# Kernel optimization log

Hardware: AMD Instinct MI355X
Metric: run time of the kernel (lower is better)

The kernel has to match this reference:

```python
import jax, jax.numpy as jnp
import numpy as np

N_MICS = 8
REF_MIC = 0
DIAG_LOAD = 1e-5
PI_ITERS = 30  # power-iteration steps for principal eigenvector of Phi_nn^-1 Phi_ss


def setup_inputs() -> dict:
    key = jax.random.key(0)
    k1, k2, k3, k4 = jax.random.split(key, 4)
    B, M, F, T = 8, N_MICS, 257, 2000
    return {
        "spec_re": jax.random.normal(k1, (B, M, F, T), dtype=jnp.float32),
        "spec_im": jax.random.normal(k2, (B, M, F, T), dtype=jnp.float32),
        "speech_mask": jax.random.uniform(k3, (B, F, T), dtype=jnp.float32),
        "noise_mask": jax.random.uniform(k4, (B, F, T), dtype=jnp.float32),
    }


def _mvdr(spec_re, spec_im, speech_mask, noise_mask):
    # (B, M, F, T) complex STFT -> (B, F, M, T) for per-(batch, freq) processing
    Y = (spec_re + 1j * spec_im).astype(jnp.complex64)
    Y = jnp.transpose(Y, (0, 2, 1, 3))  # (B, F, M, T)
    M = Y.shape[2]

    def masked_cov(mask):  # mask: (B, F, T) real
        msum = mask.sum(-1) + 1e-8                       # (B, F)
        Yw = Y * mask[:, :, None, :]                      # (B, F, M, T)
        Phi = jnp.einsum('bfmt,bfnt->bfmn', Yw, Y.conj())  # (B, F, M, M)
        return Phi / msum[..., None, None]

    Phi_ss = masked_cov(speech_mask)
    eye = jnp.eye(M, dtype=jnp.complex64)
    Phi_nn = masked_cov(noise_mask) + DIAG_LOAD * eye

    Phi_nn_inv = jnp.linalg.inv(Phi_nn)                   # batched (B, F, M, M)
    G = jnp.einsum('bfmn,bfnk->bfmk', Phi_nn_inv, Phi_ss)

    # Principal eigenvector of G via power iteration (G has real, nonnegative
    # eigenvalues since it is similar to a Hermitian-PSD generalized pencil),
    # matching torch.linalg.eig + argmax(eigenvalues.real) up to scale.
    v = jnp.ones(G.shape[:-1], dtype=jnp.complex64)       # (B, F, M)
    for _ in range(PI_ITERS):
        v = jnp.einsum('bfmn,bfn->bfm', G, v)
        v = v / (jnp.linalg.norm(v, axis=-1, keepdims=True) + 1e-12)

    # Relative transfer function normalized to reference mic (removes scale)
    rtf = v / (v[..., REF_MIC:REF_MIC + 1] + 1e-8)        # (B, F, M)

    d = jnp.einsum('bfmn,bfn->bfm', Phi_nn_inv, rtf)      # Phi_nn^-1 rtf
    denom = jnp.einsum('bfm,bfm->bf', rtf.conj(), d).real + 1e-8
    w = d / denom[..., None]                              # (B, F, M) MVDR weights

    enhanced = jnp.einsum('bfm,bfmt->bft', w.conj(), Y)   # (B, F, T) complex
    return enhanced


def reference(spec_re, spec_im, speech_mask, noise_mask):
    return _mvdr(spec_re, spec_im, speech_mask, noise_mask)
```

## Files before the change

kernel.cpp:

```cpp
#include <hip/hip_runtime.h>

#define B_DIM 8
#define M_MICS 8
#define F_DIM 257
#define T_DIM 2000
#define NPROB (B_DIM * F_DIM)

__device__ float g_w[NPROB * 16];


#define PAIR_ACC(mq, nq, k)                                             \
    {                                                                   \
        const float pr = yr[mq][u] * yr[nq][u] + yi[mq][u] * yi[nq][u]; \
        const float pi = yi[mq][u] * yr[nq][u] - yr[mq][u] * yi[nq][u]; \
        acc[(k) + 0] += msv[u] * pr;                                    \
        acc[(k) + 1] += msv[u] * pi;                                    \
        acc[(k) + 2] += mnv[u] * pr;                                    \
        acc[(k) + 3] += mnv[u] * pi;                                    \
    }

__launch_bounds__(256, 2)
__global__ void cov_solve_kernel(const float* __restrict__ sre, const float* __restrict__ sim,
                                 const float* __restrict__ smask, const float* __restrict__ nmask)
{
    const int f = blockIdx.x, b = blockIdx.y, tid = threadIdx.x;
    const int h = tid >> 6, l = tid & 63;

    __shared__ float sG[4][34];

    const size_t mrow = (size_t)F_DIM * T_DIM;
    const size_t base_bf = ((size_t)(b * M_MICS) * F_DIM + f) * T_DIM;
    const size_t mbase   = ((size_t)b * F_DIM + f) * T_DIM;

    float acc[34];
#pragma unroll
    for (int i = 0; i < 34; ++i) acc[i] = 0.f;

#pragma unroll 1
    for (int it = 0; it < 16; ++it) {
        const int t0 = 2 * l + 128 * it;
        if (t0 < T_DIM) {
            float yr[8][2], yi[8][2];
#pragma unroll
            for (int m = 0; m < 8; ++m) {
                const float2 vr = *reinterpret_cast<const float2*>(sre + base_bf + (size_t)m * mrow + t0);
                const float2 vi = *reinterpret_cast<const float2*>(sim + base_bf + (size_t)m * mrow + t0);
                yr[m][0] = vr.x; yr[m][1] = vr.y;
                yi[m][0] = vi.x; yi[m][1] = vi.y;
            }
            const float2 ms2 = *reinterpret_cast<const float2*>(smask + mbase + t0);
            const float2 mn2 = *reinterpret_cast<const float2*>(nmask + mbase + t0);
            const float msv[2] = { ms2.x, ms2.y };
            const float mnv[2] = { mn2.x, mn2.y };

            if (h == 0) {
#pragma unroll
                for (int u = 0; u < 2; ++u) {
                    acc[0] += msv[u];
                    acc[1] += mnv[u];
#pragma unroll
                    for (int m = 0; m < 8; ++m) {
                        const float pd = yr[m][u] * yr[m][u] + yi[m][u] * yi[m][u];
                        acc[2 + m]  += msv[u] * pd;
                        acc[10 + m] += mnv[u] * pd;
                    }
                    PAIR_ACC(0, 1, 18) PAIR_ACC(0, 2, 22) PAIR_ACC(0, 3, 26) PAIR_ACC(0, 4, 30)
                }
            } else if (h == 1) {
#pragma unroll
                for (int u = 0; u < 2; ++u) {
                    PAIR_ACC(0, 5, 0)  PAIR_ACC(0, 6, 4)  PAIR_ACC(0, 7, 8)  PAIR_ACC(1, 2, 12)
                    PAIR_ACC(1, 3, 16) PAIR_ACC(1, 4, 20) PAIR_ACC(1, 5, 24) PAIR_ACC(1, 6, 28)
                }
            } else if (h == 2) {
#pragma unroll
                for (int u = 0; u < 2; ++u) {
                    PAIR_ACC(1, 7, 0)  PAIR_ACC(2, 3, 4)  PAIR_ACC(2, 4, 8)  PAIR_ACC(2, 5, 12)
                    PAIR_ACC(2, 6, 16) PAIR_ACC(2, 7, 20) PAIR_ACC(3, 4, 24) PAIR_ACC(3, 5, 28)
                }
            } else {
#pragma unroll
                for (int u = 0; u < 2; ++u) {
                    PAIR_ACC(3, 6, 0)  PAIR_ACC(3, 7, 4)  PAIR_ACC(4, 5, 8)  PAIR_ACC(4, 6, 12)
                    PAIR_ACC(4, 7, 16) PAIR_ACC(5, 6, 20) PAIR_ACC(5, 7, 24) PAIR_ACC(6, 7, 28)
                }
            }
        }
    }

#pragma unroll
    for (int i = 0; i < 34; ++i) {
        acc[i] += __shfl_xor(acc[i], 1, 64);
        acc[i] += __shfl_xor(acc[i], 2, 64);
        acc[i] += __shfl_xor(acc[i], 4, 64);
        acc[i] += __shfl_xor(acc[i], 8, 64);
        acc[i] += __shfl_xor(acc[i], 16, 64);
        acc[i] += __shfl_xor(acc[i], 32, 64);
    }
    if (l == 0) {
#pragma unroll
        for (int i = 0; i < 34; ++i) sG[h][i] = acc[i];
    }
    __syncthreads();

    if (tid < 64) {
        const int r = tid >> 3, cc = tid & 7;
        const float Ssum = sG[0][0] + 1e-8f;
        const float Nsum = sG[0][1] + 1e-8f;

        float ssr, ssi, ar, ai;
        if (r == cc) {
            ssr = sG[0][2 + r] / Ssum;  ssi = 0.f;
            ar  = sG[0][10 + r] / Nsum + 1e-5f;  ai = 0.f;
        } else {
            const int mm  = (r < cc) ? r : cc;
            const int nn2 = (r < cc) ? cc : r;
            const int q = mm * 8 - mm * (mm + 1) / 2 + nn2 - mm - 1;
            const int g = (q < 4) ? 0 : (1 + ((q - 4) >> 3));
            const int basei = (q < 4) ? (18 + 4 * q) : (4 * ((q - 4) & 7));
            const float sgn = (r < cc) ? 1.f : -1.f;
            ssr = sG[g][basei] / Ssum;
            ssi = sgn * sG[g][basei + 1] / Ssum;
            ar  = sG[g][basei + 2] / Nsum;
            ai  = sgn * sG[g][basei + 3] / Nsum;
        }

        float br = (r == cc) ? 1.f : 0.f, bi = 0.f;
        for (int k = 0; k < 8; ++k) {
            const float pr = __shfl(ar, k * 9, 64);
            const float pi = __shfl(ai, k * 9, 64);
            const float den = pr * pr + pi * pi;
            const float qr = pr / den, qi = -pi / den;
            const bool isk = (r == k);
            const float ar2 = ar * qr - ai * qi;
            const float ai2 = ar * qi + ai * qr;
            const float br2 = br * qr - bi * qi;
            const float bi2 = br * qi + bi * qr;
            ar = isk ? ar2 : ar; ai = isk ? ai2 : ai;
            br = isk ? br2 : br; bi = isk ? bi2 : bi;
            const float rar = __shfl(ar, k * 8 + cc, 64);
            const float rai = __shfl(ai, k * 8 + cc, 64);
            const float rbr = __shfl(br, k * 8 + cc, 64);
            const float rbi = __shfl(bi, k * 8 + cc, 64);
            const float fr = __shfl(ar, r * 8 + k, 64);
            const float fi = __shfl(ai, r * 8 + k, 64);
            const float uar = ar - (fr * rar - fi * rai);
            const float uai = ai - (fr * rai + fi * rar);
            const float ubr = br - (fr * rbr - fi * rbi);
            const float ubi = bi - (fr * rbi + fi * rbr);
            ar = isk ? ar : uar; ai = isk ? ai : uai;
            br = isk ? br : ubr; bi = isk ? bi : ubi;
        }

        float gr = 0.f, gi = 0.f;
        for (int k = 0; k < 8; ++k) {
            const float ir = __shfl(br, r * 8 + k, 64);
            const float ii = __shfl(bi, r * 8 + k, 64);
            const float skr = __shfl(ssr, k * 8 + cc, 64);
            const float ski = __shfl(ssi, k * 8 + cc, 64);
            gr += ir * skr - ii * ski;
            gi += ir * ski + ii * skr;
        }

        float vr = 1.f, vi = 0.f;
        for (int itp = 0; itp < 30; ++itp) {
            float wr2 = gr * vr - gi * vi;
            float wi2 = gr * vi + gi * vr;
            wr2 += __shfl_xor(wr2, 1, 64); wi2 += __shfl_xor(wi2, 1, 64);
            wr2 += __shfl_xor(wr2, 2, 64); wi2 += __shfl_xor(wi2, 2, 64);
            wr2 += __shfl_xor(wr2, 4, 64); wi2 += __shfl_xor(wi2, 4, 64);
            float nrm = wr2 * wr2 + wi2 * wi2;
            nrm += __shfl_xor(nrm, 8, 64);
            nrm += __shfl_xor(nrm, 16, 64);
            nrm += __shfl_xor(nrm, 32, 64);
            const float inv = 1.f / (sqrtf(nrm) + 1e-12f);
            wr2 *= inv; wi2 *= inv;
            vr = __shfl(wr2, cc * 9, 64);
            vi = __shfl(wi2, cc * 9, 64);
        }

        const float v0r = __shfl(vr, 0, 64) + 1e-8f;
        const float v0i = __shfl(vi, 0, 64);
        const float dd = v0r * v0r + v0i * v0i;
        const float rtr = (vr * v0r + vi * v0i) / dd;
        const float rti = (vi * v0r - vr * v0i) / dd;

        float dr = br * rtr - bi * rti;
        float di = br * rti + bi * rtr;
        dr += __shfl_xor(dr, 1, 64); di += __shfl_xor(di, 1, 64);
        dr += __shfl_xor(dr, 2, 64); di += __shfl_xor(di, 2, 64);
        dr += __shfl_xor(dr, 4, 64); di += __shfl_xor(di, 4, 64);

        float qden = (r == cc) ? (rtr * dr + rti * di) : 0.f;
        qden += __shfl_xor(qden, 1, 64); qden += __shfl_xor(qden, 2, 64);
        qden += __shfl_xor(qden, 4, 64); qden += __shfl_xor(qden, 8, 64);
        qden += __shfl_xor(qden, 16, 64); qden += __shfl_xor(qden, 32, 64);
        qden += 1e-8f;

        if (cc == 0) {
            const int p = b * F_DIM + f;
            g_w[p * 16 + r]     = dr / qden;
            g_w[p * 16 + 8 + r] = di / qden;
        }
    }
}

__launch_bounds__(256, 8)
__global__ void apply_kernel(const float* __restrict__ sre, const float* __restrict__ sim,
                             float* __restrict__ out, int out_mode)
{
    const int f = blockIdx.x, b = blockIdx.y, z = blockIdx.z;
    const int tid = threadIdx.x;
    __shared__ float sW[16];
    const int p = b * F_DIM + f;
    if (tid < 16) sW[tid] = g_w[p * 16 + tid];
    __syncthreads();

    const int t0 = z * 512 + 2 * tid;
    if (t0 >= T_DIM) return;

    const size_t mrow = (size_t)F_DIM * T_DIM;
    const size_t base_bf = ((size_t)(b * M_MICS) * F_DIM + f) * T_DIM;
    const size_t mbase   = ((size_t)b * F_DIM + f) * T_DIM;

    float er0 = 0.f, ei0 = 0.f, er1 = 0.f, ei1 = 0.f;
#pragma unroll
    for (int m = 0; m < 8; ++m) {
        const float2 vr2 = *reinterpret_cast<const float2*>(sre + base_bf + (size_t)m * mrow + t0);
        const float2 vi2 = *reinterpret_cast<const float2*>(sim + base_bf + (size_t)m * mrow + t0);
        const float wr = sW[m], wi = sW[8 + m];
        er0 += wr * vr2.x + wi * vi2.x;
        ei0 += wr * vi2.x - wi * vr2.x;
        er1 += wr * vr2.y + wi * vi2.y;
        ei1 += wr * vi2.y - wi * vr2.y;
    }
    if (out_mode == 2) {
        *reinterpret_cast<float4*>(out + 2 * (mbase + t0)) = make_float4(er0, ei0, er1, ei1);
    } else {
        *reinterpret_cast<float2*>(out + mbase + t0) = make_float2(er0, er1);
    }
}

extern "C" void kernel_launch(void* const* d_in, const int* in_sizes, int n_in,
                              void* d_out, int out_size, void* d_ws, size_t ws_size,
                              hipStream_t stream)
{
    const float* sre   = (const float*)d_in[0];
    const float* sim   = (const float*)d_in[1];
    const float* smask = (const float*)d_in[2];
    const float* nmask = (const float*)d_in[3];
    float* out = (float*)d_out;

    const int mode = (out_size >= 2 * B_DIM * F_DIM * T_DIM) ? 2 : 1;

    cov_solve_kernel<<<dim3(F_DIM, B_DIM), 256, 0, stream>>>(sre, sim, smask, nmask);
    apply_kernel<<<dim3(F_DIM, B_DIM, 4), 256, 0, stream>>>(sre, sim, out, mode);
}
```

Measured before the change: 161.1 us.

## Split covariance pair accumulation across eight waves with per-wave mic subsets

The covariance kernel now runs 512 threads (8 waves) instead of 256. Wave 0 handles the mask sums and diagonal terms, and the 28 off-diagonal mic pairs are spread four per wave over the other seven waves. Those seven waves load only the mic rows they need, using float4 loads over 4 time samples. This halves accumulator registers per thread (34 to 18) and is meant to raise occupancy and memory parallelism. The cost is redundant global (likely L2-cached) reloads of mic rows across waves, plus an imbalanced wave 0 that still loops over all 8 mics with float2 loads.

Measured after the change: 174.3 us. +8.2%, slower.

```diff
diff --git a/kernel.cpp b/kernel.cpp
--- a/kernel.cpp
+++ b/kernel.cpp
@@ -9,51 +9,79 @@
 __device__ float g_w[NPROB * 16];
 
 
-#define PAIR_ACC(mq, nq, k)                                             \
+#define PAIR_ACC(a, bb, k)                                              \
     {                                                                   \
-        const float pr = yr[mq][u] * yr[nq][u] + yi[mq][u] * yi[nq][u]; \
-        const float pi = yi[mq][u] * yr[nq][u] - yr[mq][u] * yi[nq][u]; \
+        const float pr = yr[a][u] * yr[bb][u] + yi[a][u] * yi[bb][u];   \
+        const float pi = yi[a][u] * yr[bb][u] - yr[a][u] * yi[bb][u];   \
         acc[(k) + 0] += msv[u] * pr;                                    \
         acc[(k) + 1] += msv[u] * pi;                                    \
         acc[(k) + 2] += mnv[u] * pr;                                    \
         acc[(k) + 3] += mnv[u] * pi;                                    \
     }
 
-__launch_bounds__(256, 2)
+#define LOAD4(k, m)                                                                                 \
+    {                                                                                               \
+        const float4 vr_ = *reinterpret_cast<const float4*>(sre + base_bf + (size_t)(m) * mrow + t0); \
+        const float4 vi_ = *reinterpret_cast<const float4*>(sim + base_bf + (size_t)(m) * mrow + t0); \
+        yr[k][0] = vr_.x; yr[k][1] = vr_.y; yr[k][2] = vr_.z; yr[k][3] = vr_.w;                     \
+        yi[k][0] = vi_.x; yi[k][1] = vi_.y; yi[k][2] = vi_.z; yi[k][3] = vi_.w;                     \
+    }
+
+#define MASK4                                                                              \
+    const float4 ms4 = *reinterpret_cast<const float4*>(smask + mbase + t0);               \
+    const float4 mn4 = *reinterpret_cast<const float4*>(nmask + mbase + t0);               \
+    const float msv[4] = { ms4.x, ms4.y, ms4.z, ms4.w };                                   \
+    const float mnv[4] = { mn4.x, mn4.y, mn4.z, mn4.w };
+
+#define PAIR_LOOP(BODY_LOADS, BODY_ACCS, KMICS)                         \
+    {                                                                   \
+        _Pragma("unroll 1")                                             \
+        for (int it = 0; it < 8; ++it) {                                \
+            const int t0 = 4 * l + 256 * it;                            \
+            if (t0 < T_DIM) {                                           \
+                float yr[KMICS][4], yi[KMICS][4];                       \
+                BODY_LOADS                                              \
+                MASK4                                                   \
+                _Pragma("unroll")                                       \
+                for (int u = 0; u < 4; ++u) { BODY_ACCS }               \
+            }                                                           \
+        }                                                               \
+    }
+
+__launch_bounds__(512, 4)
 __global__ void cov_solve_kernel(const float* __restrict__ sre, const float* __restrict__ sim,
                                  const float* __restrict__ smask, const float* __restrict__ nmask)
 {
     const int f = blockIdx.x, b = blockIdx.y, tid = threadIdx.x;
     const int h = tid >> 6, l = tid & 63;
 
-    __shared__ float sG[4][34];
+    __shared__ float sG[8][20];
 
     const size_t mrow = (size_t)F_DIM * T_DIM;
     const size_t base_bf = ((size_t)(b * M_MICS) * F_DIM + f) * T_DIM;
     const size_t mbase   = ((size_t)b * F_DIM + f) * T_DIM;
 
-    float acc[34];
-#pragma unroll
-    for (int i = 0; i < 34; ++i) acc[i] = 0.f;
-
+    float acc[18];
+#pragma unroll
+    for (int i = 0; i < 18; ++i) acc[i] = 0.f;
+
+    if (h == 0) {
 #pragma unroll 1
-    for (int it = 0; it < 16; ++it) {
-        const int t0 = 2 * l + 128 * it;
-        if (t0 < T_DIM) {
-            float yr[8][2], yi[8][2];
-#pragma unroll
-            for (int m = 0; m < 8; ++m) {
-                const float2 vr = *reinterpret_cast<const float2*>(sre + base_bf + (size_t)m * mrow + t0);
-                const float2 vi = *reinterpret_cast<const float2*>(sim + base_bf + (size_t)m * mrow + t0);
-                yr[m][0] = vr.x; yr[m][1] = vr.y;
-                yi[m][0] = vi.x; yi[m][1] = vi.y;
-            }
-            const float2 ms2 = *reinterpret_cast<const float2*>(smask + mbase + t0);
-            const float2 mn2 = *reinterpret_cast<const float2*>(nmask + mbase + t0);
-            const float msv[2] = { ms2.x, ms2.y };
-            const float mnv[2] = { mn2.x, mn2.y };
-
-            if (h == 0) {
+        for (int it = 0; it < 16; ++it) {
+            const int t0 = 2 * l + 128 * it;
+            if (t0 < T_DIM) {
+                float yr[8][2], yi[8][2];
+#pragma unroll
+                for (int m = 0; m < 8; ++m) {
+                    const float2 vr_ = *reinterpret_cast<const float2*>(sre + base_bf + (size_t)m * mrow + t0);
+                    const float2 vi_ = *reinterpret_cast<const float2*>(sim + base_bf + (size_t)m * mrow + t0);
+                    yr[m][0] = vr_.x; yr[m][1] = vr_.y;
+                    yi[m][0] = vi_.x; yi[m][1] = vi_.y;
+                }
+                const float2 ms2 = *reinterpret_cast<const float2*>(smask + mbase + t0);
+                const float2 mn2 = *reinterpret_cast<const float2*>(nmask + mbase + t0);
+                const float msv[2] = { ms2.x, ms2.y };
+                const float mnv[2] = { mn2.x, mn2.y };
 #pragma unroll
                 for (int u = 0; u < 2; ++u) {
                     acc[0] += msv[u];
@@ -64,32 +92,34 @@
                         acc[2 + m]  += msv[u] * pd;
                         acc[10 + m] += mnv[u] * pd;
                     }
-                    PAIR_ACC(0, 1, 18) PAIR_ACC(0, 2, 22) PAIR_ACC(0, 3, 26) PAIR_ACC(0, 4, 30)
-                }
-            } else if (h == 1) {
-#pragma unroll
-                for (int u = 0; u < 2; ++u) {
-                    PAIR_ACC(0, 5, 0)  PAIR_ACC(0, 6, 4)  PAIR_ACC(0, 7, 8)  PAIR_ACC(1, 2, 12)
-                    PAIR_ACC(1, 3, 16) PAIR_ACC(1, 4, 20) PAIR_ACC(1, 5, 24) PAIR_ACC(1, 6, 28)
-                }
-            } else if (h == 2) {
-#pragma unroll
-                for (int u = 0; u < 2; ++u) {
-                    PAIR_ACC(1, 7, 0)  PAIR_ACC(2, 3, 4)  PAIR_ACC(2, 4, 8)  PAIR_ACC(2, 5, 12)
-                    PAIR_ACC(2, 6, 16) PAIR_ACC(2, 7, 20) PAIR_ACC(3, 4, 24) PAIR_ACC(3, 5, 28)
-                }
-            } else {
-#pragma unroll
-                for (int u = 0; u < 2; ++u) {
-                    PAIR_ACC(3, 6, 0)  PAIR_ACC(3, 7, 4)  PAIR_ACC(4, 5, 8)  PAIR_ACC(4, 6, 12)
-                    PAIR_ACC(4, 7, 16) PAIR_ACC(5, 6, 20) PAIR_ACC(5, 7, 24) PAIR_ACC(6, 7, 28)
                 }
             }
         }
-    }
-
-#pragma unroll
-    for (int i = 0; i < 34; ++i) {
+    } else if (h == 1) {
+        PAIR_LOOP(LOAD4(0,0) LOAD4(1,1) LOAD4(2,2) LOAD4(3,3) LOAD4(4,4),
+                  PAIR_ACC(0,1,0) PAIR_ACC(0,2,4) PAIR_ACC(0,3,8) PAIR_ACC(0,4,12), 5)
+    } else if (h == 2) {
+        PAIR_LOOP(LOAD4(0,0) LOAD4(1,1) LOAD4(2,2) LOAD4(3,5) LOAD4(4,6) LOAD4(5,7),
+                  PAIR_ACC(0,3,0) PAIR_ACC(0,4,4) PAIR_ACC(0,5,8) PAIR_ACC(1,2,12), 6)
+    } else if (h == 3) {
+        PAIR_LOOP(LOAD4(0,1) LOAD4(1,3) LOAD4(2,4) LOAD4(3,5) LOAD4(4,6),
+                  PAIR_ACC(0,1,0) PAIR_ACC(0,2,4) PAIR_ACC(0,3,8) PAIR_ACC(0,4,12), 5)
+    } else if (h == 4) {
+        PAIR_LOOP(LOAD4(0,1) LOAD4(1,2) LOAD4(2,3) LOAD4(3,4) LOAD4(4,5) LOAD4(5,7),
+                  PAIR_ACC(0,5,0) PAIR_ACC(1,2,4) PAIR_ACC(1,3,8) PAIR_ACC(1,4,12), 6)
+    } else if (h == 5) {
+        PAIR_LOOP(LOAD4(0,2) LOAD4(1,3) LOAD4(2,4) LOAD4(3,5) LOAD4(4,6) LOAD4(5,7),
+                  PAIR_ACC(0,4,0) PAIR_ACC(0,5,4) PAIR_ACC(1,2,8) PAIR_ACC(1,3,12), 6)
+    } else if (h == 6) {
+        PAIR_LOOP(LOAD4(0,3) LOAD4(1,4) LOAD4(2,5) LOAD4(3,6) LOAD4(4,7),
+                  PAIR_ACC(0,3,0) PAIR_ACC(0,4,4) PAIR_ACC(1,2,8) PAIR_ACC(1,3,12), 5)
+    } else {
+        PAIR_LOOP(LOAD4(0,4) LOAD4(1,5) LOAD4(2,6) LOAD4(3,7),
+                  PAIR_ACC(0,3,0) PAIR_ACC(1,2,4) PAIR_ACC(1,3,8) PAIR_ACC(2,3,12), 4)
+    }
+
+#pragma unroll
+    for (int i = 0; i < 18; ++i) {
         acc[i] += __shfl_xor(acc[i], 1, 64);
         acc[i] += __shfl_xor(acc[i], 2, 64);
         acc[i] += __shfl_xor(acc[i], 4, 64);
@@ -99,7 +129,7 @@
     }
     if (l == 0) {
 #pragma unroll
-        for (int i = 0; i < 34; ++i) sG[h][i] = acc[i];
+        for (int i = 0; i < 18; ++i) sG[h][i] = acc[i];
     }
     __syncthreads();
 
@@ -116,8 +146,8 @@
             const int mm  = (r < cc) ? r : cc;
             const int nn2 = (r < cc) ? cc : r;
             const int q = mm * 8 - mm * (mm + 1) / 2 + nn2 - mm - 1;
-            const int g = (q < 4) ? 0 : (1 + ((q - 4) >> 3));
-            const int basei = (q < 4) ? (18 + 4 * q) : (4 * ((q - 4) & 7));
+            const int g = 1 + (q >> 2);
+            const int basei = 4 * (q & 3);
             const float sgn = (r < cc) ? 1.f : -1.f;
             ssr = sG[g][basei] / Ssum;
             ssi = sgn * sG[g][basei + 1] / Ssum;
@@ -253,6 +283,6 @@
 
     const int mode = (out_size >= 2 * B_DIM * F_DIM * T_DIM) ? 2 : 1;
 
-    cov_solve_kernel<<<dim3(F_DIM, B_DIM), 256, 0, stream>>>(sre, sim, smask, nmask);
+    cov_solve_kernel<<<dim3(F_DIM, B_DIM), 512, 0, stream>>>(sre, sim, smask, nmask);
     apply_kernel<<<dim3(F_DIM, B_DIM, 4), 256, 0, stream>>>(sre, sim, out, mode);
 }
```
